# Performance work log

Hardware: AMD Instinct MI355X
Metric: run time of the kernel (lower is better)

## Reference

```python
import jax, jax.numpy as jnp
import numpy as np

STRIDES = (8, 16, 32, 64, 128)
SCORE_THRESH = 0.05
IOU_THRESH = 0.6
MAX_DET = 1000


def _flat(p):
    # [B,C,H,W] -> [B,H*W,C]
    B, C = p.shape[0], p.shape[1]
    return jnp.transpose(p, (0, 2, 3, 1)).reshape(B, -1, C)


def _coords(h, w, stride):
    # FCOS coords_fmap2orig: center of each stride cell, (x, y) order -> [h*w, 2]
    sx = (jnp.arange(w, dtype=jnp.float32) * stride + stride // 2)
    sy = (jnp.arange(h, dtype=jnp.float32) * stride + stride // 2)
    yy, xx = jnp.meshgrid(sy, sx, indexing='ij')
    return jnp.stack([xx.ravel(), yy.ravel()], axis=-1)


def _nms_keep(boxes, valid, thr):
    # boxes: [M,4] sorted by descending score; valid: [M] bool. Greedy NMS keep mask.
    x1, y1, x2, y2 = boxes[:, 0], boxes[:, 1], boxes[:, 2], boxes[:, 3]
    area = (x2 - x1 + 1.0) * (y2 - y1 + 1.0)
    xx1 = jnp.maximum(x1[:, None], x1[None, :])
    yy1 = jnp.maximum(y1[:, None], y1[None, :])
    xx2 = jnp.minimum(x2[:, None], x2[None, :])
    yy2 = jnp.minimum(y2[:, None], y2[None, :])
    inter = jnp.clip(xx2 - xx1, 0.0) * jnp.clip(yy2 - yy1, 0.0)
    iou = inter / (area[:, None] + area[None, :] - inter)
    M = boxes.shape[0]
    idx = jnp.arange(M)

    def body(i, keep):
        sup = (idx > i) & (iou[i] > thr) & keep[i]
        return keep & (~sup)

    return jax.lax.fori_loop(0, M, body, valid)


def setup_inputs() -> dict:
    key = jax.random.key(0)
    B, C = 16, 80
    sizes = [(128, 128), (64, 64), (32, 32), (16, 16), (8, 8)]
    ks = jax.random.split(key, 15)
    inp = {}
    for i, (h, w) in enumerate(sizes):
        lvl = i + 3
        inp[f'cls_p{lvl}'] = jax.random.normal(ks[3 * i], (B, C, h, w), jnp.float32)
        inp[f'cnt_p{lvl}'] = jax.random.normal(ks[3 * i + 1], (B, 1, h, w), jnp.float32)
        inp[f'reg_p{lvl}'] = jax.random.uniform(ks[3 * i + 2], (B, 4, h, w), jnp.float32) * 100.0
    return inp


def _detect(cls_levels, cnt_levels, reg_levels):
    cls_logits = jnp.concatenate([_flat(p) for p in cls_levels], axis=1)  # [B,N,80]
    cnt_logits = jnp.concatenate([_flat(p) for p in cnt_levels], axis=1)  # [B,N,1]
    reg_preds = jnp.concatenate([_flat(p) for p in reg_levels], axis=1)   # [B,N,4]
    coords = jnp.concatenate(
        [_coords(p.shape[2], p.shape[3], s) for p, s in zip(cls_levels, STRIDES)], axis=0)  # [N,2]

    cls_preds = jax.nn.sigmoid(cls_logits)
    cnt_preds = jax.nn.sigmoid(cnt_logits)[..., 0]                        # [B,N]
    cls_max = jnp.max(cls_preds, axis=-1)                                 # [B,N]
    cls_classes = jnp.argmax(cls_preds, axis=-1) + 1                      # [B,N] 1-based labels
    scores = jnp.sqrt(cls_max * cnt_preds)                                # add_centerness

    boxes = jnp.concatenate(
        [coords[None] - reg_preds[..., :2], coords[None] + reg_preds[..., 2:]], axis=-1)  # [B,N,4]

    M = min(MAX_DET, scores.shape[1])
    topv, topi = jax.lax.top_k(scores, M)                                 # sorted desc
    classes_k = jnp.take_along_axis(cls_classes, topi, axis=1)            # [B,M]
    boxes_k = jnp.take_along_axis(boxes, topi[..., None], axis=1)         # [B,M,4]
    valid = topv >= SCORE_THRESH

    def per_image(b, s, c, v):
        # class-aware NMS via coordinate offset trick
        off = c.astype(b.dtype) * (jnp.max(b) + 1.0)
        keep = _nms_keep(b + off[:, None], v, IOU_THRESH)
        kf = keep.astype(s.dtype)
        return s * kf, c * keep.astype(c.dtype), b * kf[:, None]

    return jax.vmap(per_image)(boxes_k, topv, classes_k, valid)


def reference(cls_p3, cnt_p3, reg_p3, cls_p4, cnt_p4, reg_p4, cls_p5, cnt_p5, reg_p5,
              cls_p6, cnt_p6, reg_p6, cls_p7, cnt_p7, reg_p7):
    cls_levels = [cls_p3, cls_p4, cls_p5, cls_p6, cls_p7]
    cnt_levels = [cnt_p3, cnt_p4, cnt_p5, cnt_p6, cnt_p7]
    reg_levels = [reg_p3, reg_p4, reg_p5, reg_p6, reg_p7]
    return _detect(cls_levels, cnt_levels, reg_levels)
```

## Files before the change

### kernel.cpp

```cpp
#include <hip/hip_runtime.h>
#include <hip/hip_bf16.h>
#include <math.h>

#define NB 16
#define NC 80
#define NA 21824
#define NM 1000
#define NHBINS 2048
#define CANDCAP 4096

#define OFF_KEYS     0ul
#define OFF_CLSV     2793472ul
#define OFF_HIST     4190208ul
#define OFF_CANDCNT  4321280ul
#define OFF_MAXB     4321344ul
#define OFF_CANDS    4321408ul
#define OFF_TOPSCORE 4845696ul
#define OFF_TOPCLS   4909696ul
#define OFF_TOPBOX   4973696ul
#define OFF_MASK     5229696ul

__device__ __forceinline__ float sigm(float x) { return 1.0f / (1.0f + expf(-x)); }

__global__ __launch_bounds__(256, 6) void k_score(
    const float* __restrict__ cls3, const float* __restrict__ cnt3,
    const float* __restrict__ cls4, const float* __restrict__ cnt4,
    const float* __restrict__ cls5, const float* __restrict__ cnt5,
    const float* __restrict__ cls6, const float* __restrict__ cnt6,
    const float* __restrict__ cls7, const float* __restrict__ cnt7,
    unsigned long long* __restrict__ keys,
    float* __restrict__ clsv, unsigned int* __restrict__ hist)
{
    __shared__ unsigned int histpk[NHBINS / 2];
    __shared__ float lm[4 * 64 * 4];
    __shared__ int   lam[4 * 64 * 4];
    __shared__ float cm[256];
    __shared__ int   cam[256];
    const int b = blockIdx.y;
    const int tid = threadIdx.x;
    const int a = tid & 63, s = tid >> 6;
    const int g4 = blockIdx.x * 64 + a;

    for (int i = tid; i < NHBINS / 2; i += 256) histpk[i] = 0u;

    if (g4 < (NA >> 2)) {
        const int n = g4 << 2;
        const float* clsP; int off, logW;
        if      (n < 16384) { clsP = cls3; off = 0;     logW = 7; }
        else if (n < 20480) { clsP = cls4; off = 16384; logW = 6; }
        else if (n < 21504) { clsP = cls5; off = 20480; logW = 5; }
        else if (n < 21760) { clsP = cls6; off = 21504; logW = 4; }
        else                { clsP = cls7; off = 21760; logW = 3; }
        const int HW4 = 1 << (2 * logW - 2);
        const int l4 = (n - off) >> 2;
        const float4* cp = (const float4*)clsP + (size_t)b * NC * HW4 + l4;
        const int c0 = s * 20;
        float4 buf[4];
#pragma unroll
        for (int u = 0; u < 4; u++) buf[u] = cp[(size_t)(c0 + u) * HW4];
        float m[4] = { -3.402823466e+38f, -3.402823466e+38f, -3.402823466e+38f, -3.402823466e+38f };
        int am[4] = { c0, c0, c0, c0 };
#pragma unroll
        for (int u = 0; u < 20; u++) {
            float4 vv = buf[u & 3];
            if (u + 4 < 20) buf[u & 3] = cp[(size_t)(c0 + u + 4) * HW4];
            const int c = c0 + u;
            if (vv.x > m[0]) { m[0] = vv.x; am[0] = c; }
            if (vv.y > m[1]) { m[1] = vv.y; am[1] = c; }
            if (vv.z > m[2]) { m[2] = vv.z; am[2] = c; }
            if (vv.w > m[3]) { m[3] = vv.w; am[3] = c; }
        }
#pragma unroll
        for (int k = 0; k < 4; k++) { lm[tid * 4 + k] = m[k]; lam[tid * 4 + k] = am[k]; }
    }
    __syncthreads();
    if (tid < 64 && (blockIdx.x * 64 + tid) < (NA >> 2)) {
        float M[4]; int AM[4];
#pragma unroll
        for (int k = 0; k < 4; k++) { M[k] = lm[tid * 4 + k]; AM[k] = lam[tid * 4 + k]; }
        for (int s2 = 1; s2 < 4; s2++) {
#pragma unroll
            for (int k = 0; k < 4; k++) {
                float vv = lm[(s2 * 64 + tid) * 4 + k];
                if (vv > M[k]) { M[k] = vv; AM[k] = lam[(s2 * 64 + tid) * 4 + k]; }
            }
        }
#pragma unroll
        for (int k = 0; k < 4; k++) { cm[tid * 4 + k] = M[k]; cam[tid * 4 + k] = AM[k]; }
    }
    __syncthreads();
    const int n2 = blockIdx.x * 256 + tid;
    if (n2 < NA) {
        const float* cntP; int off, logW;
        if      (n2 < 16384) { cntP = cnt3; off = 0;     logW = 7; }
        else if (n2 < 20480) { cntP = cnt4; off = 16384; logW = 6; }
        else if (n2 < 21504) { cntP = cnt5; off = 20480; logW = 5; }
        else if (n2 < 21760) { cntP = cnt6; off = 21504; logW = 4; }
        else                 { cntP = cnt7; off = 21760; logW = 3; }
        const int HW = 1 << (2 * logW);
        const int local = n2 - off;
        float cn = cntP[(size_t)b * HW + local];
        float M = cm[tid]; int AM = cam[tid];
        float sc = sqrtf(sigm(M) * sigm(cn));
        unsigned long long key = ((unsigned long long)__float_as_uint(sc) << 32)
                               | (unsigned int)(~(unsigned int)n2);
        keys[(size_t)b * NA + n2] = key;
        unsigned int bin = (unsigned int)(key >> 51);
        atomicAdd(&histpk[bin >> 1], (bin & 1u) ? 0x10000u : 1u);
        clsv[(size_t)b * NA + n2] = (float)(AM + 1);
    }
    __syncthreads();
    unsigned int* gh = hist + b * NHBINS;
    for (int i = tid; i < NHBINS / 2; i += 256) {
        unsigned int pk = histpk[i];
        if (pk) {
            unsigned int lo = pk & 0xFFFFu, hi = pk >> 16;
            if (lo) atomicAdd(&gh[2 * i], lo);
            if (hi) atomicAdd(&gh[2 * i + 1], hi);
        }
    }
}

__global__ __launch_bounds__(256) void k_compact(
    const unsigned long long* __restrict__ keys, const unsigned int* __restrict__ hist,
    unsigned int* __restrict__ candcnt, unsigned long long* __restrict__ cands)
{
    __shared__ int part1[256];
    __shared__ int part2[8];
    __shared__ int sBoundary;
    __shared__ unsigned int lcount;
    __shared__ unsigned int lbase;
    const int b = blockIdx.y;
    const int tid = threadIdx.x;
    const unsigned int* h = hist + b * NHBINS;
    int sum = 0;
    for (int i = 0; i < 8; i++) sum += (int)h[tid * 8 + i];
    part1[tid] = sum;
    if (tid == 0) lcount = 0u;
    __syncthreads();
    if (tid < 8) { int s2 = 0; for (int t = 0; t < 32; t++) s2 += part1[tid * 32 + t]; part2[tid] = s2; }
    __syncthreads();
    if (tid == 0) {
        int acc = 0, sc;
        for (sc = 7; sc > 0; sc--) { if (acc + part2[sc] >= NM) break; acc += part2[sc]; }
        int t;
        for (t = sc * 32 + 31; t > sc * 32; t--) { if (acc + part1[t] >= NM) break; acc += part1[t]; }
        int bin;
        for (bin = t * 8 + 7; bin > t * 8; bin--) { if (acc + (int)h[bin] >= NM) break; acc += (int)h[bin]; }
        sBoundary = bin;
    }
    __syncthreads();
    const unsigned int boundary = (unsigned int)sBoundary;
    unsigned long long hk[4]; unsigned int hslot[4]; int nh = 0;
    for (int nn = blockIdx.x * 256 + tid; nn < NA; nn += 22 * 256) {
        unsigned long long key = keys[(size_t)b * NA + nn];
        if ((unsigned int)(key >> 51) >= boundary) {
            hslot[nh] = atomicAdd(&lcount, 1u);
            hk[nh] = key;
            nh++;
        }
    }
    __syncthreads();
    if (tid == 0) lbase = atomicAdd(&candcnt[b], lcount);
    __syncthreads();
    const unsigned int base = lbase;
    for (int t = 0; t < nh; t++) {
        unsigned int pos = base + hslot[t];
        if (pos < CANDCAP) cands[(size_t)b * CANDCAP + pos] = hk[t];
    }
}

__global__ __launch_bounds__(256) void k_rank(
    const unsigned long long* __restrict__ cands, const unsigned int* __restrict__ candcnt,
    const float* __restrict__ clsv,
    const float* __restrict__ reg3, const float* __restrict__ reg4, const float* __restrict__ reg5,
    const float* __restrict__ reg6, const float* __restrict__ reg7,
    float* __restrict__ topscore, float* __restrict__ topcls,
    float4* __restrict__ topbox, unsigned int* __restrict__ maxbEnc)
{
    __shared__ unsigned long long sbuf[CANDCAP];
    __shared__ unsigned int redmax[256];
    const int b = blockIdx.y;
    int cnt = (int)candcnt[b]; if (cnt > CANDCAP) cnt = CANDCAP;
    const int base = blockIdx.x * 256;
    if (base >= cnt) return;
    const int tid = threadIdx.x;
    for (int i = tid; i < cnt; i += 256) sbuf[i] = cands[(size_t)b * CANDCAP + i];
    __syncthreads();
    const int idx = base + tid;
    unsigned int enc = 0;
    if (idx < cnt) {
        const unsigned long long key = sbuf[idx];
        const unsigned int ai = ~(unsigned int)key;
        const float* regP; int off, W, logW, st;
        if      (ai < 16384) { regP = reg3; off = 0;     W = 128; logW = 7; st = 8;   }
        else if (ai < 20480) { regP = reg4; off = 16384; W = 64;  logW = 6; st = 16;  }
        else if (ai < 21504) { regP = reg5; off = 20480; W = 32;  logW = 5; st = 32;  }
        else if (ai < 21760) { regP = reg6; off = 21504; W = 16;  logW = 4; st = 64;  }
        else                 { regP = reg7; off = 21760; W = 8;   logW = 3; st = 128; }
        const int local = (int)ai - off;
        const int HW = 1 << (2 * logW);
        const float* rp = regP + (size_t)b * 4 * HW + local;
        float r0 = rp[0], r1 = rp[HW], r2 = rp[2 * HW], r3 = rp[3 * HW];
        float cv = clsv[(size_t)b * NA + ai];
        int rank = 0;
        int j = 0;
        for (; j + 4 <= cnt; j += 4) {
            rank += (sbuf[j] > key) + (sbuf[j+1] > key) + (sbuf[j+2] > key) + (sbuf[j+3] > key);
        }
        for (; j < cnt; j++) rank += (sbuf[j] > key);
        if (rank < NM) {
            const float hs = (float)(st >> 1);
            float cx = (float)((local & (W - 1)) * st) + hs;
            float cy = (float)((local >> logW) * st) + hs;
            float4 bx = make_float4(cx - r0, cy - r1, cx + r2, cy + r3);
            topscore[b * NM + rank] = __uint_as_float((unsigned int)(key >> 32));
            topcls[b * NM + rank] = cv;
            topbox[b * NM + rank] = bx;
            float mx = fmaxf(fmaxf(bx.x, bx.y), fmaxf(bx.z, bx.w));
            unsigned int ub = __float_as_uint(mx);
            enc = (ub & 0x80000000u) ? ~ub : (ub | 0x80000000u);
        }
    }
    redmax[tid] = enc;
    __syncthreads();
    for (int sgap = 128; sgap > 0; sgap >>= 1) {
        if (tid < sgap) { unsigned int o = redmax[tid + sgap]; if (o > redmax[tid]) redmax[tid] = o; }
        __syncthreads();
    }
    if (tid == 0 && redmax[0]) atomicMax(&maxbEnc[b], redmax[0]);
}

__global__ __launch_bounds__(256) void k_iou(
    const float4* __restrict__ topbox, const float* __restrict__ topcls,
    const unsigned int* __restrict__ maxbEnc, unsigned long long* __restrict__ maskArr)
{
    __shared__ float4 sB[NM];
    __shared__ float sA[NM];
    const int b = blockIdx.y;
    const int tid = threadIdx.x;
    unsigned int enc = maxbEnc[b];
    unsigned int ub = (enc & 0x80000000u) ? (enc & 0x7FFFFFFFu) : ~enc;
    const float mp1 = __fadd_rn(__uint_as_float(ub), 1.0f);
    for (int r = tid; r < NM; r += 256) {
        float4 f = topbox[b * NM + r];
        float off = __fmul_rn(topcls[b * NM + r], mp1);
        f.x = __fadd_rn(f.x, off); f.y = __fadd_rn(f.y, off);
        f.z = __fadd_rn(f.z, off); f.w = __fadd_rn(f.w, off);
        sB[r] = f;
        sA[r] = __fmul_rn(__fadd_rn(__fsub_rn(f.z, f.x), 1.0f),
                          __fadd_rn(__fsub_rn(f.w, f.y), 1.0f));
    }
    __syncthreads();
    int task = blockIdx.x * 256 + tid;
    if (task >= NM * 16) return;
    int w = task / NM, i = task - w * NM;
    float4 bi = sB[i]; float ai = sA[i];
    unsigned long long bits = 0ULL;
    int j0 = w << 6;
    int jstart = (j0 > i + 1) ? j0 : i + 1;
    int jend = (j0 + 64 < NM) ? j0 + 64 : NM;
    for (int j = jstart; j < jend; j++) {
        float4 bj = sB[j];
        float xx1 = fmaxf(bi.x, bj.x);
        float yy1 = fmaxf(bi.y, bj.y);
        float xx2 = fminf(bi.z, bj.z);
        float yy2 = fminf(bi.w, bj.w);
        float iw = fmaxf(__fsub_rn(xx2, xx1), 0.0f);
        float ih = fmaxf(__fsub_rn(yy2, yy1), 0.0f);
        float inter = __fmul_rn(iw, ih);
        float denom = __fsub_rn(__fadd_rn(ai, sA[j]), inter);
        float iou = inter / denom;
        if (iou > 0.6f) bits |= (1ULL << (j - j0));
    }
    maskArr[((size_t)b * 16 + w) * NM + i] = bits;
}

__global__ __launch_bounds__(256) void k_nms_sweep(
    const unsigned long long* __restrict__ maskArr,
    const float* __restrict__ topscore, const float* __restrict__ topcls,
    const float4* __restrict__ topbox, float* __restrict__ out)
{
    __shared__ unsigned long long smask[16 * NM];
    __shared__ unsigned long long lremv[16];
    const int b = blockIdx.x;
    const int tid = threadIdx.x;
    const int j = tid & 63, q = tid >> 6;
    const unsigned long long* gmask = maskArr + (size_t)b * (16 * NM);

    {
        const ulonglong2* src = (const ulonglong2*)gmask;
        ulonglong2* dst = (ulonglong2*)smask;
        for (int idx = tid; idx < 8 * NM; idx += 256) dst[idx] = src[idx];
    }
    if (tid < 16) lremv[tid] = 0ULL;
    __syncthreads();
    for (int r = tid; r < NM; r += 256) {
        float s = topscore[b * NM + r];
        if (!(s >= 0.05f)) atomicOr(&lremv[r >> 6], 1ULL << (r & 63));
    }

    for (int w = 0; w < 16; w++) {
        __syncthreads();
        const int row = w * 64 + j;
        unsigned long long D = (row < NM) ? smask[w * NM + row] : 0ULL;
        unsigned int dlo = (unsigned int)D, dhi = (unsigned int)(D >> 32);
        unsigned long long sv = lremv[w];
        unsigned int slo = __builtin_amdgcn_readfirstlane((unsigned int)sv);
        unsigned int shi = __builtin_amdgcn_readfirstlane((unsigned int)(sv >> 32));
        unsigned long long s = ((unsigned long long)shi << 32) | slo;
#pragma unroll
        for (int bb = 0; bb < 64; bb++) {
            unsigned int rlo = __builtin_amdgcn_readlane(dlo, bb);
            unsigned int rhi = __builtin_amdgcn_readlane(dhi, bb);
            unsigned long long rowv = ((unsigned long long)rhi << 32) | rlo;
            unsigned long long t = s | rowv;
            s = ((s >> bb) & 1ULL) ? s : t;
        }
        if (tid == 0) lremv[w] = s;
        const unsigned long long kw = ~s;
        if ((kw >> j) & 1ULL) {
            for (int k = w + 1 + q; k < 16; k += 4) {
                unsigned long long v = (row < NM) ? smask[k * NM + row] : 0ULL;
                if (v) atomicOr(&lremv[k], v);
            }
        }
    }
    __syncthreads();

    for (int r = tid; r < NM; r += 256) {
        bool keep = !((lremv[r >> 6] >> (r & 63)) & 1ULL);
        float kf = keep ? 1.0f : 0.0f;
        out[b * NM + r] = topscore[b * NM + r] * kf;
        out[NB * NM + b * NM + r] = topcls[b * NM + r] * kf;
        float4 bx = topbox[b * NM + r];
        ((float4*)(out + 2 * NB * NM))[b * NM + r] = make_float4(bx.x * kf, bx.y * kf, bx.z * kf, bx.w * kf);
    }
}

extern "C" void kernel_launch(void* const* d_in, const int* in_sizes, int n_in,
                              void* d_out, int out_size, void* d_ws, size_t ws_size,
                              hipStream_t stream) {
    const float* cls3 = (const float*)d_in[0];
    const float* cnt3 = (const float*)d_in[1];
    const float* reg3 = (const float*)d_in[2];
    const float* cls4 = (const float*)d_in[3];
    const float* cnt4 = (const float*)d_in[4];
    const float* reg4 = (const float*)d_in[5];
    const float* cls5 = (const float*)d_in[6];
    const float* cnt5 = (const float*)d_in[7];
    const float* reg5 = (const float*)d_in[8];
    const float* cls6 = (const float*)d_in[9];
    const float* cnt6 = (const float*)d_in[10];
    const float* reg6 = (const float*)d_in[11];
    const float* cls7 = (const float*)d_in[12];
    const float* cnt7 = (const float*)d_in[13];
    const float* reg7 = (const float*)d_in[14];

    char* ws = (char*)d_ws;
    unsigned long long* keys   = (unsigned long long*)(ws + OFF_KEYS);
    float*              clsv   = (float*)(ws + OFF_CLSV);
    unsigned int*       hist   = (unsigned int*)(ws + OFF_HIST);
    unsigned int*       candcnt= (unsigned int*)(ws + OFF_CANDCNT);
    unsigned int*       maxbE  = (unsigned int*)(ws + OFF_MAXB);
    unsigned long long* cands  = (unsigned long long*)(ws + OFF_CANDS);
    float*              topsc  = (float*)(ws + OFF_TOPSCORE);
    float*              topcl  = (float*)(ws + OFF_TOPCLS);
    float4*             topbx  = (float4*)(ws + OFF_TOPBOX);
    unsigned long long* maskA  = (unsigned long long*)(ws + OFF_MASK);

    hipMemsetAsync(ws + OFF_HIST, 0, (size_t)(NB * NHBINS * 4 + 128), stream);

    dim3 g1(86, NB);
    k_score<<<g1, 256, 0, stream>>>(cls3, cnt3, cls4, cnt4, cls5, cnt5,
                                    cls6, cnt6, cls7, cnt7,
                                    keys, clsv, hist);
    dim3 g2(22, NB);
    k_compact<<<g2, 256, 0, stream>>>(keys, hist, candcnt, cands);
    dim3 g3(CANDCAP / 256, NB);
    k_rank<<<g3, 256, 0, stream>>>(cands, candcnt, clsv, reg3, reg4, reg5, reg6, reg7,
                                   topsc, topcl, topbx, maxbE);
    dim3 g4(63, NB);
    k_iou<<<g4, 256, 0, stream>>>(topbx, topcl, maxbE, maskA);
    k_nms_sweep<<<NB, 256, 0, stream>>>(maskA, topsc, topcl, topbx, (float*)d_out);
}
```

Before: 266.0 us.

## Fuse histogram, compaction and ranking into one per-image selection kernel

Removes the global histogram from the score kernel, along with the memset and the separate compact and rank kernels. A single block per image now builds the histogram in shared memory, finds the top-k boundary, scatters candidates into bin-sorted order and ranks each one only within its own bin. This drops two launches, the memset and the global atomics, and cuts the rank comparisons from all candidates to one bin. The cost is that each image is handled by one 256-thread block, so only 16 blocks run and each rereads the key array twice serially.

```diff
diff --git a/kernel.cpp b/kernel.cpp
--- a/kernel.cpp
+++ b/kernel.cpp
@@ -1,5 +1,4 @@
 #include <hip/hip_runtime.h>
-#include <hip/hip_bf16.h>
 #include <math.h>
 
 #define NB 16
@@ -11,14 +10,11 @@
 
 #define OFF_KEYS     0ul
 #define OFF_CLSV     2793472ul
-#define OFF_HIST     4190208ul
-#define OFF_CANDCNT  4321280ul
-#define OFF_MAXB     4321344ul
-#define OFF_CANDS    4321408ul
-#define OFF_TOPSCORE 4845696ul
-#define OFF_TOPCLS   4909696ul
-#define OFF_TOPBOX   4973696ul
-#define OFF_MASK     5229696ul
+#define OFF_TOPSCORE 4190208ul
+#define OFF_TOPCLS   4254208ul
+#define OFF_TOPBOX   4318208ul
+#define OFF_MAXB     4574208ul
+#define OFF_MASK     4574272ul
 
 __device__ __forceinline__ float sigm(float x) { return 1.0f / (1.0f + expf(-x)); }
 
@@ -29,9 +25,8 @@
     const float* __restrict__ cls6, const float* __restrict__ cnt6,
     const float* __restrict__ cls7, const float* __restrict__ cnt7,
     unsigned long long* __restrict__ keys,
-    float* __restrict__ clsv, unsigned int* __restrict__ hist)
+    float* __restrict__ clsv)
 {
-    __shared__ unsigned int histpk[NHBINS / 2];
     __shared__ float lm[4 * 64 * 4];
     __shared__ int   lam[4 * 64 * 4];
     __shared__ float cm[256];
@@ -40,8 +35,6 @@
     const int tid = threadIdx.x;
     const int a = tid & 63, s = tid >> 6;
     const int g4 = blockIdx.x * 64 + a;
-
-    for (int i = tid; i < NHBINS / 2; i += 256) histpk[i] = 0u;
 
     if (g4 < (NA >> 2)) {
         const int n = g4 << 2;
@@ -105,143 +98,127 @@
         unsigned long long key = ((unsigned long long)__float_as_uint(sc) << 32)
                                | (unsigned int)(~(unsigned int)n2);
         keys[(size_t)b * NA + n2] = key;
-        unsigned int bin = (unsigned int)(key >> 51);
-        atomicAdd(&histpk[bin >> 1], (bin & 1u) ? 0x10000u : 1u);
         clsv[(size_t)b * NA + n2] = (float)(AM + 1);
     }
-    __syncthreads();
-    unsigned int* gh = hist + b * NHBINS;
-    for (int i = tid; i < NHBINS / 2; i += 256) {
-        unsigned int pk = histpk[i];
-        if (pk) {
-            unsigned int lo = pk & 0xFFFFu, hi = pk >> 16;
-            if (lo) atomicAdd(&gh[2 * i], lo);
-            if (hi) atomicAdd(&gh[2 * i + 1], hi);
-        }
-    }
-}
-
-__global__ __launch_bounds__(256) void k_compact(
-    const unsigned long long* __restrict__ keys, const unsigned int* __restrict__ hist,
-    unsigned int* __restrict__ candcnt, unsigned long long* __restrict__ cands)
+}
+
+__global__ __launch_bounds__(256) void k_mid(
+    const unsigned long long* __restrict__ keys, const float* __restrict__ clsv,
+    const float* __restrict__ reg3, const float* __restrict__ reg4, const float* __restrict__ reg5,
+    const float* __restrict__ reg6, const float* __restrict__ reg7,
+    float* __restrict__ topscore, float* __restrict__ topcls,
+    float4* __restrict__ topbox, float* __restrict__ maxb)
 {
+    __shared__ unsigned int sh_hist[NHBINS];
+    __shared__ unsigned int sh_cur[NHBINS];
+    __shared__ unsigned int sh_off[NHBINS];
+    __shared__ unsigned long long scand[CANDCAP];
     __shared__ int part1[256];
     __shared__ int part2[8];
     __shared__ int sBoundary;
-    __shared__ unsigned int lcount;
-    __shared__ unsigned int lbase;
-    const int b = blockIdx.y;
+    __shared__ float redmax[256];
+
+    const int b = blockIdx.x;
     const int tid = threadIdx.x;
-    const unsigned int* h = hist + b * NHBINS;
-    int sum = 0;
-    for (int i = 0; i < 8; i++) sum += (int)h[tid * 8 + i];
-    part1[tid] = sum;
-    if (tid == 0) lcount = 0u;
+    const unsigned long long* kb = keys + (size_t)b * NA;
+    const ulonglong2* k2 = (const ulonglong2*)kb;
+
+    for (int i = tid; i < NHBINS; i += 256) { sh_hist[i] = 0u; sh_cur[i] = 0u; }
+    __syncthreads();
+
+    for (int i = tid; i < NA / 2; i += 256) {
+        ulonglong2 v = k2[i];
+        atomicAdd(&sh_hist[(unsigned int)(v.x >> 51)], 1u);
+        atomicAdd(&sh_hist[(unsigned int)(v.y >> 51)], 1u);
+    }
+    __syncthreads();
+
+    { int s = 0; for (int i = 0; i < 8; i++) s += (int)sh_hist[tid * 8 + i]; part1[tid] = s; }
     __syncthreads();
     if (tid < 8) { int s2 = 0; for (int t = 0; t < 32; t++) s2 += part1[tid * 32 + t]; part2[tid] = s2; }
     __syncthreads();
+
     if (tid == 0) {
         int acc = 0, sc;
         for (sc = 7; sc > 0; sc--) { if (acc + part2[sc] >= NM) break; acc += part2[sc]; }
         int t;
         for (t = sc * 32 + 31; t > sc * 32; t--) { if (acc + part1[t] >= NM) break; acc += part1[t]; }
         int bin;
-        for (bin = t * 8 + 7; bin > t * 8; bin--) { if (acc + (int)h[bin] >= NM) break; acc += (int)h[bin]; }
+        for (bin = t * 8 + 7; bin > t * 8; bin--) { if (acc + (int)sh_hist[bin] >= NM) break; acc += (int)sh_hist[bin]; }
         sBoundary = bin;
     }
-    __syncthreads();
+    {
+        const int g = tid >> 5;
+        int acc = 0;
+        for (int q = g + 1; q < 8; q++) acc += part2[q];
+        for (int t2 = (g << 5) + 31; t2 > tid; t2--) acc += part1[t2];
+        int run = acc;
+        for (int k = 7; k >= 0; k--) { sh_off[tid * 8 + k] = (unsigned int)run; run += (int)sh_hist[tid * 8 + k]; }
+    }
+    __syncthreads();
+
     const unsigned int boundary = (unsigned int)sBoundary;
-    unsigned long long hk[4]; unsigned int hslot[4]; int nh = 0;
-    for (int nn = blockIdx.x * 256 + tid; nn < NA; nn += 22 * 256) {
-        unsigned long long key = keys[(size_t)b * NA + nn];
-        if ((unsigned int)(key >> 51) >= boundary) {
-            hslot[nh] = atomicAdd(&lcount, 1u);
-            hk[nh] = key;
-            nh++;
-        }
-    }
-    __syncthreads();
-    if (tid == 0) lbase = atomicAdd(&candcnt[b], lcount);
-    __syncthreads();
-    const unsigned int base = lbase;
-    for (int t = 0; t < nh; t++) {
-        unsigned int pos = base + hslot[t];
-        if (pos < CANDCAP) cands[(size_t)b * CANDCAP + pos] = hk[t];
-    }
-}
-
-__global__ __launch_bounds__(256) void k_rank(
-    const unsigned long long* __restrict__ cands, const unsigned int* __restrict__ candcnt,
-    const float* __restrict__ clsv,
-    const float* __restrict__ reg3, const float* __restrict__ reg4, const float* __restrict__ reg5,
-    const float* __restrict__ reg6, const float* __restrict__ reg7,
-    float* __restrict__ topscore, float* __restrict__ topcls,
-    float4* __restrict__ topbox, unsigned int* __restrict__ maxbEnc)
-{
-    __shared__ unsigned long long sbuf[CANDCAP];
-    __shared__ unsigned int redmax[256];
-    const int b = blockIdx.y;
-    int cnt = (int)candcnt[b]; if (cnt > CANDCAP) cnt = CANDCAP;
-    const int base = blockIdx.x * 256;
-    if (base >= cnt) return;
-    const int tid = threadIdx.x;
-    for (int i = tid; i < cnt; i += 256) sbuf[i] = cands[(size_t)b * CANDCAP + i];
-    __syncthreads();
-    const int idx = base + tid;
-    unsigned int enc = 0;
-    if (idx < cnt) {
-        const unsigned long long key = sbuf[idx];
-        const unsigned int ai = ~(unsigned int)key;
-        const float* regP; int off, W, logW, st;
-        if      (ai < 16384) { regP = reg3; off = 0;     W = 128; logW = 7; st = 8;   }
-        else if (ai < 20480) { regP = reg4; off = 16384; W = 64;  logW = 6; st = 16;  }
-        else if (ai < 21504) { regP = reg5; off = 20480; W = 32;  logW = 5; st = 32;  }
-        else if (ai < 21760) { regP = reg6; off = 21504; W = 16;  logW = 4; st = 64;  }
-        else                 { regP = reg7; off = 21760; W = 8;   logW = 3; st = 128; }
-        const int local = (int)ai - off;
-        const int HW = 1 << (2 * logW);
-        const float* rp = regP + (size_t)b * 4 * HW + local;
-        float r0 = rp[0], r1 = rp[HW], r2 = rp[2 * HW], r3 = rp[3 * HW];
-        float cv = clsv[(size_t)b * NA + ai];
-        int rank = 0;
-        int j = 0;
-        for (; j + 4 <= cnt; j += 4) {
-            rank += (sbuf[j] > key) + (sbuf[j+1] > key) + (sbuf[j+2] > key) + (sbuf[j+3] > key);
-        }
-        for (; j < cnt; j++) rank += (sbuf[j] > key);
+    int cnt = (int)(sh_off[boundary] + sh_hist[boundary]);
+    if (cnt > CANDCAP) cnt = CANDCAP;
+
+    for (int i = tid; i < NA / 2; i += 256) {
+        ulonglong2 v = k2[i];
+        unsigned int b0 = (unsigned int)(v.x >> 51);
+        if (b0 >= boundary) { unsigned int p = sh_off[b0] + atomicAdd(&sh_cur[b0], 1u); if (p < CANDCAP) scand[p] = v.x; }
+        unsigned int b1 = (unsigned int)(v.y >> 51);
+        if (b1 >= boundary) { unsigned int p = sh_off[b1] + atomicAdd(&sh_cur[b1], 1u); if (p < CANDCAP) scand[p] = v.y; }
+    }
+    __syncthreads();
+
+    float mymax = -3.402823466e+38f;
+    for (int idx = tid; idx < cnt; idx += 256) {
+        const unsigned long long key = scand[idx];
+        const unsigned int bin = (unsigned int)(key >> 51);
+        int seg0 = (int)sh_off[bin];
+        int seg1 = seg0 + (int)sh_hist[bin]; if (seg1 > cnt) seg1 = cnt;
+        int rank = seg0;
+        for (int j = seg0; j < seg1; j++) rank += (scand[j] > key);
         if (rank < NM) {
+            const unsigned int ai = ~(unsigned int)key;
+            const float* regP; int lvloff, W, logW, st;
+            if      (ai < 16384) { regP = reg3; lvloff = 0;     W = 128; logW = 7; st = 8;   }
+            else if (ai < 20480) { regP = reg4; lvloff = 16384; W = 64;  logW = 6; st = 16;  }
+            else if (ai < 21504) { regP = reg5; lvloff = 20480; W = 32;  logW = 5; st = 32;  }
+            else if (ai < 21760) { regP = reg6; lvloff = 21504; W = 16;  logW = 4; st = 64;  }
+            else                 { regP = reg7; lvloff = 21760; W = 8;   logW = 3; st = 128; }
+            const int local = (int)ai - lvloff;
+            const int HW = 1 << (2 * logW);
+            const float* rp = regP + (size_t)b * 4 * HW + local;
+            float r0 = rp[0], r1 = rp[HW], r2 = rp[2 * HW], r3 = rp[3 * HW];
+            float cv = clsv[(size_t)b * NA + ai];
             const float hs = (float)(st >> 1);
             float cx = (float)((local & (W - 1)) * st) + hs;
             float cy = (float)((local >> logW) * st) + hs;
-            float4 bx = make_float4(cx - r0, cy - r1, cx + r2, cy + r3);
+            float4 bxv = make_float4(cx - r0, cy - r1, cx + r2, cy + r3);
             topscore[b * NM + rank] = __uint_as_float((unsigned int)(key >> 32));
             topcls[b * NM + rank] = cv;
-            topbox[b * NM + rank] = bx;
-            float mx = fmaxf(fmaxf(bx.x, bx.y), fmaxf(bx.z, bx.w));
-            unsigned int ub = __float_as_uint(mx);
-            enc = (ub & 0x80000000u) ? ~ub : (ub | 0x80000000u);
-        }
-    }
-    redmax[tid] = enc;
+            topbox[b * NM + rank] = bxv;
+            mymax = fmaxf(mymax, fmaxf(fmaxf(bxv.x, bxv.y), fmaxf(bxv.z, bxv.w)));
+        }
+    }
+    redmax[tid] = mymax;
     __syncthreads();
     for (int sgap = 128; sgap > 0; sgap >>= 1) {
-        if (tid < sgap) { unsigned int o = redmax[tid + sgap]; if (o > redmax[tid]) redmax[tid] = o; }
+        if (tid < sgap) redmax[tid] = fmaxf(redmax[tid], redmax[tid + sgap]);
         __syncthreads();
     }
-    if (tid == 0 && redmax[0]) atomicMax(&maxbEnc[b], redmax[0]);
+    if (tid == 0) maxb[b] = __fadd_rn(redmax[0], 1.0f);
 }
 
 __global__ __launch_bounds__(256) void k_iou(
     const float4* __restrict__ topbox, const float* __restrict__ topcls,
-    const unsigned int* __restrict__ maxbEnc, unsigned long long* __restrict__ maskArr)
+    const float* __restrict__ maxb, unsigned long long* __restrict__ maskArr)
 {
     __shared__ float4 sB[NM];
     __shared__ float sA[NM];
     const int b = blockIdx.y;
     const int tid = threadIdx.x;
-    unsigned int enc = maxbEnc[b];
-    unsigned int ub = (enc & 0x80000000u) ? (enc & 0x7FFFFFFFu) : ~enc;
-    const float mp1 = __fadd_rn(__uint_as_float(ub), 1.0f);
+    const float mp1 = maxb[b];
     for (int r = tid; r < NM; r += 256) {
         float4 f = topbox[b * NM + r];
         float off = __fmul_rn(topcls[b * NM + r], mp1);
@@ -360,27 +337,20 @@
     char* ws = (char*)d_ws;
     unsigned long long* keys   = (unsigned long long*)(ws + OFF_KEYS);
     float*              clsv   = (float*)(ws + OFF_CLSV);
-    unsigned int*       hist   = (unsigned int*)(ws + OFF_HIST);
-    unsigned int*       candcnt= (unsigned int*)(ws + OFF_CANDCNT);
-    unsigned int*       maxbE  = (unsigned int*)(ws + OFF_MAXB);
-    unsigned long long* cands  = (unsigned long long*)(ws + OFF_CANDS);
     float*              topsc  = (float*)(ws + OFF_TOPSCORE);
     float*              topcl  = (float*)(ws + OFF_TOPCLS);
     float4*             topbx  = (float4*)(ws + OFF_TOPBOX);
+    float*              maxbF  = (float*)(ws + OFF_MAXB);
     unsigned long long* maskA  = (unsigned long long*)(ws + OFF_MASK);
 
-    hipMemsetAsync(ws + OFF_HIST, 0, (size_t)(NB * NHBINS * 4 + 128), stream);
 
     dim3 g1(86, NB);
     k_score<<<g1, 256, 0, stream>>>(cls3, cnt3, cls4, cnt4, cls5, cnt5,
                                     cls6, cnt6, cls7, cnt7,
-                                    keys, clsv, hist);
-    dim3 g2(22, NB);
-    k_compact<<<g2, 256, 0, stream>>>(keys, hist, candcnt, cands);
-    dim3 g3(CANDCAP / 256, NB);
-    k_rank<<<g3, 256, 0, stream>>>(cands, candcnt, clsv, reg3, reg4, reg5, reg6, reg7,
-                                   topsc, topcl, topbx, maxbE);
+                                    keys, clsv);
+    k_mid<<<dim3(NB), 256, 0, stream>>>(keys, clsv, reg3, reg4, reg5, reg6, reg7,
+                                        topsc, topcl, topbx, maxbF);
     dim3 g4(63, NB);
-    k_iou<<<g4, 256, 0, stream>>>(topbx, topcl, maxbE, maskA);
+    k_iou<<<g4, 256, 0, stream>>>(topbx, topcl, maxbF, maskA);
     k_nms_sweep<<<NB, 256, 0, stream>>>(maskA, topsc, topcl, topbx, (float*)d_out);
 }
```

Result: slower. 421.1 us (+58.3%).
